# Kernel optimization log

Hardware: AMD Instinct MI355X
Metric: run time of the kernel (lower is better)

## Reference

```python
import jax, jax.numpy as jnp
import numpy as np

WS = 7       # window size
SHIFT = 3    # shift size (ws // 2)
NH = 8       # num heads


def _make_swin_mask(Hp, Wp, ws, shift):
    # Standard Swin attn mask for shifted windows: (nW, ws*ws, ws*ws)
    img = np.zeros((Hp, Wp), dtype=np.float32)
    cnt = 0
    for hs in (slice(0, -ws), slice(-ws, -shift), slice(-shift, None)):
        for wsl in (slice(0, -ws), slice(-ws, -shift), slice(-shift, None)):
            img[hs, wsl] = cnt
            cnt += 1
    mw = img.reshape(Hp // ws, ws, Wp // ws, ws).transpose(0, 2, 1, 3).reshape(-1, ws * ws)
    diff = mw[:, None, :] - mw[:, :, None]
    return jnp.asarray(np.where(diff != 0, -100.0, 0.0).astype(np.float32))


def setup_inputs() -> dict:
    key = jax.random.key(0)
    ks = jax.random.split(key, 5)
    B, H, W, C = 8, 128, 128, 256
    pad = (WS - H % WS) % WS
    Hp, Wp = H + pad, W + pad  # 133, 133
    x = jax.random.normal(ks[0], (B, H * W, C), dtype=jnp.float32)
    qkv_w = jax.random.normal(ks[1], (3 * C, C), dtype=jnp.float32) * 0.02
    qkv_b = jax.random.normal(ks[2], (3 * C,), dtype=jnp.float32) * 0.02
    proj_w = jax.random.normal(ks[3], (C, C), dtype=jnp.float32) * 0.02
    proj_b = jax.random.normal(ks[4], (C,), dtype=jnp.float32) * 0.02
    mask_matrix = _make_swin_mask(Hp, Wp, WS, SHIFT)
    return {"x": x, "qkv_w": qkv_w, "qkv_b": qkv_b, "proj_w": proj_w,
            "proj_b": proj_b, "mask_matrix": mask_matrix, "H": H, "W": W}


def reference(x, qkv_w, qkv_b, proj_w, proj_b, mask_matrix, H, W):
    B, N, C = x.shape
    hd = C // NH
    scale = hd ** -0.5
    xg = x.reshape(B, H, W, C)
    pad_r = (WS - W % WS) % WS
    pad_b = (WS - H % WS) % WS
    xg = jnp.pad(xg, ((0, 0), (0, pad_b), (0, pad_r), (0, 0)))
    Hp, Wp = H + pad_b, W + pad_r
    xg = jnp.roll(xg, (-SHIFT, -SHIFT), axis=(1, 2))
    h, w = Hp // WS, Wp // WS
    nW = h * w
    wsws = WS * WS
    # window partition -> (B*nW, wsws, C)
    xw = xg.reshape(B, h, WS, w, WS, C).transpose(0, 1, 3, 2, 4, 5).reshape(B * nW, wsws, C)
    qkv = xw @ qkv_w.T + qkv_b                       # (B*nW, wsws, 3C)
    qkv = qkv.reshape(B * nW, wsws, 3, NH, hd).transpose(2, 0, 3, 1, 4)
    q, k, v = qkv[0], qkv[1], qkv[2]                 # (B*nW, NH, wsws, hd)
    attn = jnp.einsum('bhqd,bhkd->bhqk', q, k) * scale
    attn = attn.reshape(B, nW, NH, wsws, wsws) + mask_matrix[None, :, None]
    attn = jax.nn.softmax(attn, axis=-1).reshape(B * nW, NH, wsws, wsws)
    out = jnp.einsum('bhqk,bhkd->bhqd', attn, v)
    out = out.transpose(0, 2, 1, 3).reshape(B * nW, wsws, C)
    out = out @ proj_w.T + proj_b
    # window reverse -> (B, Hp, Wp, C)
    out = out.reshape(B, h, w, WS, WS, C).transpose(0, 1, 3, 2, 4, 5).reshape(B, Hp, Wp, C)
    out = jnp.roll(out, (SHIFT, SHIFT), axis=(1, 2))
    return out[:, :H, :W, :].reshape(B, N, C)
```

## Files before the change

kernel.cpp:

```cpp
#include <hip/hip_runtime.h>
#include <hip/hip_bf16.h>
#include <cstdint>
#include <cstddef>

#define WS7    7
#define NHEADS 8
#define HD     32
#define CDIM   256
#define HP     133
#define NWY    19
#define NWIN   361
#define BATCH  8
#define HIMG   128
#define TOK    49
#define MTOK   64

typedef __attribute__((ext_vector_type(8))) short short8;
typedef __attribute__((ext_vector_type(4))) short short4v;
typedef __attribute__((ext_vector_type(4))) float f32x4;

#define XROW 264
#define VROW 72
#define VT_OFF     33792
#define SMEM_BYTES 70656

__device__ __forceinline__ short f2bf(float f) {
  union { float f; uint32_t u; } v; v.f = f;
  uint32_t r = v.u + 0x7FFFu + ((v.u >> 16) & 1u);
  return (short)(r >> 16);
}

#if defined(__has_builtin)
#if __has_builtin(__builtin_amdgcn_mfma_f32_16x16x16bf16_1k)
#define HAVE_MFMA16 1
#endif
#endif

__device__ __forceinline__ f32x4 mfma16(short4v a, short4v b, f32x4 c) {
#ifdef HAVE_MFMA16
  return __builtin_amdgcn_mfma_f32_16x16x16bf16_1k(a, b, c, 0, 0, 0);
#else
  asm("v_mfma_f32_16x16x16_bf16 %0, %1, %2, %0" : "+v"(c) : "v"(a), "v"(b));
  return c;
#endif
}

__device__ __forceinline__ short4v cvt4(f32x4 v, f32x4 b, float sc) {
  return (short4v){ f2bf((v[0] + b[0]) * sc), f2bf((v[1] + b[1]) * sc),
                    f2bf((v[2] + b[2]) * sc), f2bf((v[3] + b[3]) * sc) };
}

__device__ __forceinline__ int regcode(int c) { return (c < 126) ? 0 : ((c < 130) ? 1 : 2); }

__global__ void cvt_weights(const float* __restrict__ qkv_w, const float* __restrict__ proj_w,
                            short* __restrict__ qkvw_bf, short* __restrict__ projw_bf) {
  int stride = gridDim.x * blockDim.x;
  int i0 = blockIdx.x * blockDim.x + threadIdx.x;
  for (int i = i0; i < 768 * 256; i += stride) qkvw_bf[i] = f2bf(qkv_w[i]);
  for (int i = i0; i < 256 * 256; i += stride) projw_bf[i] = f2bf(proj_w[i]);
}

__global__ __launch_bounds__(512, 4) void swin_fused(
    const float* __restrict__ x, const short* __restrict__ qkvw,
    const float* __restrict__ qkv_b, const short* __restrict__ projw,
    const float* __restrict__ proj_b, float* __restrict__ out)
{
  extern __shared__ char smem[];
  const int tid  = threadIdx.x;
  const int wave = tid >> 6;
  const int lane = tid & 63;
  const int lg   = lane >> 4;
  const int ln   = lane & 15;
  const int blk  = blockIdx.x;
  const int b    = blk / NWIN;
  const int wdx  = blk - b * NWIN;
  const int wy   = wdx / NWY;
  const int wx   = wdx - wy * NWY;

  for (int i = tid; i < MTOK * 64; i += 512) {
    int r  = i >> 6;
    int c4 = i & 63;
    short4v v = (short4v){0, 0, 0, 0};
    if (r < TOK) {
      int ty = r / WS7, tx = r - (r / WS7) * WS7;
      int sh = wy * WS7 + ty + 3; if (sh >= HP) sh -= HP;
      int sw = wx * WS7 + tx + 3; if (sw >= HP) sw -= HP;
      if (sh < HIMG && sw < HIMG) {
        const float4* p = reinterpret_cast<const float4*>(
            x + (((size_t)b * (HIMG * HIMG) + (size_t)sh * HIMG + sw) * CDIM + c4 * 4));
        float4 f = *p;
        v = (short4v){f2bf(f.x), f2bf(f.y), f2bf(f.z), f2bf(f.w)};
      }
    }
    *reinterpret_cast<short4v*>(smem + ((size_t)r * XROW + c4 * 4) * 2) = v;
  }
  __syncthreads();

  const int h = wave;
  const int qcol = h * HD;
  const int kcol = 256 + h * HD;
  const int vcol = 512 + h * HD;
  const float scale = 0.17677669529663687f;

  f32x4 acc[2][4];
  short4v qf[2][4], kf[2][4];

#pragma unroll
  for (int ct = 0; ct < 2; ++ct)
#pragma unroll
    for (int tt = 0; tt < 4; ++tt) acc[ct][tt] = (f32x4){0, 0, 0, 0};
#pragma unroll 2
  for (int ks = 0; ks < 8; ++ks) {
    int k0 = ks * 32 + lg * 8;
    short8 xb[4];
#pragma unroll
    for (int tt = 0; tt < 4; ++tt)
      xb[tt] = *reinterpret_cast<const short8*>(smem + ((16 * tt + ln) * XROW + k0) * 2);
    short8 w[2];
#pragma unroll
    for (int ct = 0; ct < 2; ++ct)
      w[ct] = *reinterpret_cast<const short8*>(qkvw + (size_t)(qcol + 16 * ct + ln) * CDIM + k0);
#pragma unroll
    for (int ct = 0; ct < 2; ++ct)
#pragma unroll
      for (int tt = 0; tt < 4; ++tt)
        acc[ct][tt] = __builtin_amdgcn_mfma_f32_16x16x32_bf16(w[ct], xb[tt], acc[ct][tt], 0, 0, 0);
  }
#pragma unroll
  for (int ct = 0; ct < 2; ++ct) {
    f32x4 bias = *reinterpret_cast<const f32x4*>(qkv_b + qcol + 16 * ct + 4 * lg);
#pragma unroll
    for (int tt = 0; tt < 4; ++tt) qf[ct][tt] = cvt4(acc[ct][tt], bias, scale);
  }

#pragma unroll
  for (int ct = 0; ct < 2; ++ct)
#pragma unroll
    for (int tt = 0; tt < 4; ++tt) acc[ct][tt] = (f32x4){0, 0, 0, 0};
#pragma unroll 2
  for (int ks = 0; ks < 8; ++ks) {
    int k0 = ks * 32 + lg * 8;
    short8 xb[4];
#pragma unroll
    for (int tt = 0; tt < 4; ++tt)
      xb[tt] = *reinterpret_cast<const short8*>(smem + ((16 * tt + ln) * XROW + k0) * 2);
    short8 w[2];
#pragma unroll
    for (int ct = 0; ct < 2; ++ct)
      w[ct] = *reinterpret_cast<const short8*>(qkvw + (size_t)(kcol + 16 * ct + ln) * CDIM + k0);
#pragma unroll
    for (int ct = 0; ct < 2; ++ct)
#pragma unroll
      for (int tt = 0; tt < 4; ++tt)
        acc[ct][tt] = __builtin_amdgcn_mfma_f32_16x16x32_bf16(w[ct], xb[tt], acc[ct][tt], 0, 0, 0);
  }
#pragma unroll
  for (int ct = 0; ct < 2; ++ct) {
    f32x4 bias = *reinterpret_cast<const f32x4*>(qkv_b + kcol + 16 * ct + 4 * lg);
#pragma unroll
    for (int tt = 0; tt < 4; ++tt) kf[ct][tt] = cvt4(acc[ct][tt], bias, 1.0f);
  }

#pragma unroll
  for (int ct = 0; ct < 2; ++ct)
#pragma unroll
    for (int tt = 0; tt < 4; ++tt) acc[ct][tt] = (f32x4){0, 0, 0, 0};
#pragma unroll 2
  for (int ks = 0; ks < 8; ++ks) {
    int k0 = ks * 32 + lg * 8;
    short8 xb[4];
#pragma unroll
    for (int tt = 0; tt < 4; ++tt)
      xb[tt] = *reinterpret_cast<const short8*>(smem + ((16 * tt + ln) * XROW + k0) * 2);
    short8 w[2];
#pragma unroll
    for (int ct = 0; ct < 2; ++ct)
      w[ct] = *reinterpret_cast<const short8*>(qkvw + (size_t)(vcol + 16 * ct + ln) * CDIM + k0);
#pragma unroll
    for (int ct = 0; ct < 2; ++ct)
#pragma unroll
      for (int tt = 0; tt < 4; ++tt)
        acc[ct][tt] = __builtin_amdgcn_mfma_f32_16x16x32_bf16(w[ct], xb[tt], acc[ct][tt], 0, 0, 0);
  }
#pragma unroll
  for (int ct = 0; ct < 2; ++ct) {
    f32x4 bias = *reinterpret_cast<const f32x4*>(qkv_b + vcol + 16 * ct + 4 * lg);
#pragma unroll
    for (int tt = 0; tt < 4; ++tt)
#pragma unroll
      for (int r = 0; r < 4; ++r) {
        int row = h * HD + 16 * ct + 4 * lg + r;
        int col = 16 * tt + ln;
        *reinterpret_cast<short*>(smem + VT_OFF + (row * VROW + col) * 2) =
            f2bf(acc[ct][tt][r] + bias[r]);
      }
  }
  __syncthreads();

  f32x4 s[4][4];
#pragma unroll
  for (int kt = 0; kt < 4; ++kt)
#pragma unroll
    for (int qt = 0; qt < 4; ++qt) s[kt][qt] = (f32x4){0, 0, 0, 0};
#pragma unroll
  for (int step = 0; step < 2; ++step)
#pragma unroll
    for (int kt = 0; kt < 4; ++kt)
#pragma unroll
      for (int qt = 0; qt < 4; ++qt)
        s[kt][qt] = mfma16(kf[step][kt], qf[step][qt], s[kt][qt]);

  const bool bnd = (wy == NWY - 1) || (wx == NWY - 1);
  short4v pf[4][4];
#pragma unroll
  for (int qt = 0; qt < 4; ++qt) {
    int q = 16 * qt + ln;
    int qcode = 0;
    if (bnd) {
      int qy = (q * 37) >> 8, qx = q - 7 * qy;
      qcode = 3 * regcode(wy * WS7 + qy) + regcode(wx * WS7 + qx);
    }
#pragma unroll
    for (int kt = 0; kt < 4; ++kt)
#pragma unroll
      for (int r = 0; r < 4; ++r) {
        int key = 16 * kt + 4 * lg + r;
        float v = s[kt][qt][r];
        if (bnd) {
          int ky = (key * 37) >> 8, kx = key - 7 * ky;
          int kc = 3 * regcode(wy * WS7 + ky) + regcode(wx * WS7 + kx);
          if (kc != qcode) v -= 100.0f;
        }
        if (key >= TOK) v = -1e30f;
        s[kt][qt][r] = v;
      }
    float m = -1e30f;
#pragma unroll
    for (int kt = 0; kt < 4; ++kt)
#pragma unroll
      for (int r = 0; r < 4; ++r) m = fmaxf(m, s[kt][qt][r]);
    m = fmaxf(m, __shfl_xor(m, 16));
    m = fmaxf(m, __shfl_xor(m, 32));
    float sum = 0.f;
#pragma unroll
    for (int kt = 0; kt < 4; ++kt)
#pragma unroll
      for (int r = 0; r < 4; ++r) {
        float e = __expf(s[kt][qt][r] - m);
        s[kt][qt][r] = e; sum += e;
      }
    sum += __shfl_xor(sum, 16);
    sum += __shfl_xor(sum, 32);
    float inv = 1.0f / sum;
#pragma unroll
    for (int kt = 0; kt < 4; ++kt)
      pf[kt][qt] = (short4v){ f2bf(s[kt][qt][0] * inv), f2bf(s[kt][qt][1] * inv),
                              f2bf(s[kt][qt][2] * inv), f2bf(s[kt][qt][3] * inv) };
  }

  f32x4 o[4][2];
#pragma unroll
  for (int qt = 0; qt < 4; ++qt)
#pragma unroll
    for (int n2 = 0; n2 < 2; ++n2) o[qt][n2] = (f32x4){0, 0, 0, 0};
#pragma unroll
  for (int kt = 0; kt < 4; ++kt) {
    short4v vb0 = *reinterpret_cast<const short4v*>(
        smem + VT_OFF + ((h * HD + ln) * VROW + 16 * kt + 4 * lg) * 2);
    short4v vb1 = *reinterpret_cast<const short4v*>(
        smem + VT_OFF + ((h * HD + 16 + ln) * VROW + 16 * kt + 4 * lg) * 2);
#pragma unroll
    for (int qt = 0; qt < 4; ++qt) {
      o[qt][0] = mfma16(pf[kt][qt], vb0, o[qt][0]);
      o[qt][1] = mfma16(pf[kt][qt], vb1, o[qt][1]);
    }
  }

#pragma unroll
  for (int qt = 0; qt < 4; ++qt)
#pragma unroll
    for (int n2 = 0; n2 < 2; ++n2)
#pragma unroll
      for (int r = 0; r < 4; ++r) {
        int row = 16 * qt + 4 * lg + r;
        int col = h * HD + 16 * n2 + ln;
        *reinterpret_cast<short*>(smem + (row * XROW + col) * 2) = f2bf(o[qt][n2][r]);
      }
  __syncthreads();

  f32x4 pacc[4][2];
#pragma unroll
  for (int mt = 0; mt < 4; ++mt)
#pragma unroll
    for (int n2 = 0; n2 < 2; ++n2) pacc[mt][n2] = (f32x4){0, 0, 0, 0};
#pragma unroll 2
  for (int ks = 0; ks < 8; ++ks) {
    int k0 = ks * 32 + lg * 8;
    short8 afr[4];
#pragma unroll
    for (int mt = 0; mt < 4; ++mt)
      afr[mt] = *reinterpret_cast<const short8*>(smem + ((16 * mt + ln) * XROW + k0) * 2);
    short8 bfr[2];
#pragma unroll
    for (int n2 = 0; n2 < 2; ++n2)
      bfr[n2] = *reinterpret_cast<const short8*>(projw + (size_t)(h * HD + 16 * n2 + ln) * CDIM + k0);
#pragma unroll
    for (int n2 = 0; n2 < 2; ++n2)
#pragma unroll
      for (int mt = 0; mt < 4; ++mt)
        pacc[mt][n2] = __builtin_amdgcn_mfma_f32_16x16x32_bf16(afr[mt], bfr[n2], pacc[mt][n2], 0, 0, 0);
  }

  float pb0 = proj_b[h * HD + ln];
  float pb1 = proj_b[h * HD + 16 + ln];
#pragma unroll
  for (int mt = 0; mt < 4; ++mt)
#pragma unroll
    for (int r = 0; r < 4; ++r) {
      int t = 16 * mt + 4 * lg + r;
      if (t < TOK) {
        int ty = t / WS7, tx = t - (t / WS7) * WS7;
        int sh = wy * WS7 + ty + 3; if (sh >= HP) sh -= HP;
        int sw = wx * WS7 + tx + 3; if (sw >= HP) sw -= HP;
        if (sh < HIMG && sw < HIMG) {
          float* po = out + ((size_t)b * (HIMG * HIMG) + (size_t)sh * HIMG + sw) * CDIM + h * HD + ln;
          po[0]  = pacc[mt][0][r] + pb0;
          po[16] = pacc[mt][1][r] + pb1;
        }
      }
    }
}

extern "C" void kernel_launch(void* const* d_in, const int* in_sizes, int n_in,
                              void* d_out, int out_size, void* d_ws, size_t ws_size,
                              hipStream_t stream) {
  const float* x      = (const float*)d_in[0];
  const float* qkv_w  = (const float*)d_in[1];
  const float* qkv_b  = (const float*)d_in[2];
  const float* proj_w = (const float*)d_in[3];
  const float* proj_b = (const float*)d_in[4];
  float* out          = (float*)d_out;

  short* qkvw_bf = (short*)d_ws;
  short* projw_bf = (short*)((char*)d_ws + 768 * 256 * 2);

  hipLaunchKernelGGL(cvt_weights, dim3(256), dim3(256), 0, stream,
                     qkv_w, proj_w, qkvw_bf, projw_bf);

  hipFuncSetAttribute((const void*)swin_fused,
                      hipFuncAttributeMaxDynamicSharedMemorySize, SMEM_BYTES);
  hipLaunchKernelGGL(swin_fused, dim3(BATCH * NWIN), dim3(512), SMEM_BYTES, stream,
                     x, qkvw_bf, qkv_b, projw_bf, proj_b, out);
}
```

Baseline: 273.7 us.

## Use packed bf16 conversion, exp2 softmax, and permuted V and output layouts

Replaces scalar bf16 rounding with the packed hardware conversion, and folds log2(e) into the query scale and mask constant so softmax can use exp2. Restructures the x load so each wave loads whole rows. Changes the V transpose padding and interleaves head-dim columns so the attention output is written as packed 32-bit stores. The aim is fewer conversion and exponent instructions and fewer shared-memory stores, at the cost of a more intricate column permutation that must stay consistent across stages.

```diff
diff --git a/kernel.cpp b/kernel.cpp
--- a/kernel.cpp
+++ b/kernel.cpp
@@ -14,21 +14,41 @@
 #define HIMG   128
 #define TOK    49
 #define MTOK   64
+#define SHIFT3 3
 
 typedef __attribute__((ext_vector_type(8))) short short8;
 typedef __attribute__((ext_vector_type(4))) short short4v;
 typedef __attribute__((ext_vector_type(4))) float f32x4;
 
-#define XROW 264
-#define VROW 72
-#define VT_OFF     33792
-#define SMEM_BYTES 70656
+#define XROWB  528
+#define VROW   76
+#define VT_OFF 33792
+#define SMEM_BYTES (VT_OFF + 256*VROW*2)
+
+#define QS      0.25505653712988137f
+#define MASKL2 -144.26950408889634f
 
 __device__ __forceinline__ short f2bf(float f) {
   union { float f; uint32_t u; } v; v.f = f;
   uint32_t r = v.u + 0x7FFFu + ((v.u >> 16) & 1u);
   return (short)(r >> 16);
 }
+
+__device__ __forceinline__ uint32_t pk2(float a, float b) {
+  union { __hip_bfloat162 h; uint32_t u; } cv;
+  cv.h = __float22bfloat162_rn(float2{a, b});
+  return cv.u;
+}
+
+#if defined(__has_builtin)
+#if __has_builtin(__builtin_amdgcn_exp2f)
+#define EXP2F __builtin_amdgcn_exp2f
+#else
+#define EXP2F exp2f
+#endif
+#else
+#define EXP2F exp2f
+#endif
 
 #if defined(__has_builtin)
 #if __has_builtin(__builtin_amdgcn_mfma_f32_16x16x16bf16_1k)
@@ -43,11 +63,6 @@
   asm("v_mfma_f32_16x16x16_bf16 %0, %1, %2, %0" : "+v"(c) : "v"(a), "v"(b));
   return c;
 #endif
-}
-
-__device__ __forceinline__ short4v cvt4(f32x4 v, f32x4 b, float sc) {
-  return (short4v){ f2bf((v[0] + b[0]) * sc), f2bf((v[1] + b[1]) * sc),
-                    f2bf((v[2] + b[2]) * sc), f2bf((v[3] + b[3]) * sc) };
 }
 
 __device__ __forceinline__ int regcode(int c) { return (c < 126) ? 0 : ((c < 130) ? 1 : 2); }
@@ -77,22 +92,24 @@
   const int wy   = wdx / NWY;
   const int wx   = wdx - wy * NWY;
 
-  for (int i = tid; i < MTOK * 64; i += 512) {
-    int r  = i >> 6;
-    int c4 = i & 63;
-    short4v v = (short4v){0, 0, 0, 0};
-    if (r < TOK) {
-      int ty = r / WS7, tx = r - (r / WS7) * WS7;
-      int sh = wy * WS7 + ty + 3; if (sh >= HP) sh -= HP;
-      int sw = wx * WS7 + tx + 3; if (sw >= HP) sw -= HP;
-      if (sh < HIMG && sw < HIMG) {
-        const float4* p = reinterpret_cast<const float4*>(
-            x + (((size_t)b * (HIMG * HIMG) + (size_t)sh * HIMG + sw) * CDIM + c4 * 4));
-        float4 f = *p;
-        v = (short4v){f2bf(f.x), f2bf(f.y), f2bf(f.z), f2bf(f.w)};
+  {
+    const int c4 = lane;
+#pragma unroll
+    for (int it = 0; it < 8; ++it) {
+      int r = 8 * it + wave;
+      uint2 v = make_uint2(0u, 0u);
+      if (r < TOK) {
+        int ty = r / WS7, tx = r - WS7 * (r / WS7);
+        int sh = wy * WS7 + ty + SHIFT3; if (sh >= HP) sh -= HP;
+        int sw = wx * WS7 + tx + SHIFT3; if (sw >= HP) sw -= HP;
+        if (sh < HIMG && sw < HIMG) {
+          const float4 f = *reinterpret_cast<const float4*>(
+              x + (((size_t)b * (HIMG * HIMG) + sh * HIMG + sw) * CDIM + c4 * 4));
+          v = make_uint2(pk2(f.x, f.y), pk2(f.z, f.w));
+        }
       }
-    }
-    *reinterpret_cast<short4v*>(smem + ((size_t)r * XROW + c4 * 4) * 2) = v;
+      *reinterpret_cast<uint2*>(smem + r * XROWB + c4 * 8) = v;
+    }
   }
   __syncthreads();
 
@@ -100,100 +117,78 @@
   const int qcol = h * HD;
   const int kcol = 256 + h * HD;
   const int vcol = 512 + h * HD;
-  const float scale = 0.17677669529663687f;
 
   f32x4 acc[2][4];
   short4v qf[2][4], kf[2][4];
 
-#pragma unroll
-  for (int ct = 0; ct < 2; ++ct)
-#pragma unroll
-    for (int tt = 0; tt < 4; ++tt) acc[ct][tt] = (f32x4){0, 0, 0, 0};
-#pragma unroll 2
-  for (int ks = 0; ks < 8; ++ks) {
-    int k0 = ks * 32 + lg * 8;
-    short8 xb[4];
-#pragma unroll
-    for (int tt = 0; tt < 4; ++tt)
-      xb[tt] = *reinterpret_cast<const short8*>(smem + ((16 * tt + ln) * XROW + k0) * 2);
-    short8 w[2];
-#pragma unroll
-    for (int ct = 0; ct < 2; ++ct)
-      w[ct] = *reinterpret_cast<const short8*>(qkvw + (size_t)(qcol + 16 * ct + ln) * CDIM + k0);
-#pragma unroll
-    for (int ct = 0; ct < 2; ++ct)
-#pragma unroll
-      for (int tt = 0; tt < 4; ++tt)
-        acc[ct][tt] = __builtin_amdgcn_mfma_f32_16x16x32_bf16(w[ct], xb[tt], acc[ct][tt], 0, 0, 0);
-  }
+#define QKV_PASS(COLBASE)                                                          \
+  _Pragma("unroll")                                                                \
+  for (int ct = 0; ct < 2; ++ct)                                                   \
+    _Pragma("unroll")                                                              \
+    for (int tt = 0; tt < 4; ++tt) acc[ct][tt] = (f32x4){0, 0, 0, 0};              \
+  _Pragma("unroll 2")                                                              \
+  for (int ks = 0; ks < 8; ++ks) {                                                 \
+    const int k0 = ks * 32 + lg * 8;                                               \
+    short8 xb[4];                                                                  \
+    _Pragma("unroll")                                                              \
+    for (int tt = 0; tt < 4; ++tt)                                                 \
+      xb[tt] = *reinterpret_cast<const short8*>(smem + (16 * tt + ln) * XROWB + k0 * 2); \
+    short8 w[2];                                                                   \
+    _Pragma("unroll")                                                              \
+    for (int ct = 0; ct < 2; ++ct)                                                 \
+      w[ct] = *reinterpret_cast<const short8*>(qkvw + (size_t)((COLBASE) + 16 * ct + ln) * CDIM + k0); \
+    _Pragma("unroll")                                                              \
+    for (int ct = 0; ct < 2; ++ct)                                                 \
+      _Pragma("unroll")                                                            \
+      for (int tt = 0; tt < 4; ++tt)                                               \
+        acc[ct][tt] = __builtin_amdgcn_mfma_f32_16x16x32_bf16(w[ct], xb[tt], acc[ct][tt], 0, 0, 0); \
+  }
+
+  QKV_PASS(qcol)
 #pragma unroll
   for (int ct = 0; ct < 2; ++ct) {
     f32x4 bias = *reinterpret_cast<const f32x4*>(qkv_b + qcol + 16 * ct + 4 * lg);
 #pragma unroll
-    for (int tt = 0; tt < 4; ++tt) qf[ct][tt] = cvt4(acc[ct][tt], bias, scale);
-  }
-
-#pragma unroll
-  for (int ct = 0; ct < 2; ++ct)
-#pragma unroll
-    for (int tt = 0; tt < 4; ++tt) acc[ct][tt] = (f32x4){0, 0, 0, 0};
-#pragma unroll 2
-  for (int ks = 0; ks < 8; ++ks) {
-    int k0 = ks * 32 + lg * 8;
-    short8 xb[4];
-#pragma unroll
-    for (int tt = 0; tt < 4; ++tt)
-      xb[tt] = *reinterpret_cast<const short8*>(smem + ((16 * tt + ln) * XROW + k0) * 2);
-    short8 w[2];
-#pragma unroll
-    for (int ct = 0; ct < 2; ++ct)
-      w[ct] = *reinterpret_cast<const short8*>(qkvw + (size_t)(kcol + 16 * ct + ln) * CDIM + k0);
-#pragma unroll
-    for (int ct = 0; ct < 2; ++ct)
-#pragma unroll
-      for (int tt = 0; tt < 4; ++tt)
-        acc[ct][tt] = __builtin_amdgcn_mfma_f32_16x16x32_bf16(w[ct], xb[tt], acc[ct][tt], 0, 0, 0);
-  }
+    for (int tt = 0; tt < 4; ++tt) {
+      float e0 = fmaf(acc[ct][tt][0], QS, bias[0] * QS);
+      float e1 = fmaf(acc[ct][tt][1], QS, bias[1] * QS);
+      float e2 = fmaf(acc[ct][tt][2], QS, bias[2] * QS);
+      float e3 = fmaf(acc[ct][tt][3], QS, bias[3] * QS);
+      union { uint2 u; short4v s; } cv;
+      cv.u = make_uint2(pk2(e0, e1), pk2(e2, e3));
+      qf[ct][tt] = cv.s;
+    }
+  }
+
+  QKV_PASS(kcol)
 #pragma unroll
   for (int ct = 0; ct < 2; ++ct) {
     f32x4 bias = *reinterpret_cast<const f32x4*>(qkv_b + kcol + 16 * ct + 4 * lg);
 #pragma unroll
-    for (int tt = 0; tt < 4; ++tt) kf[ct][tt] = cvt4(acc[ct][tt], bias, 1.0f);
-  }
-
-#pragma unroll
-  for (int ct = 0; ct < 2; ++ct)
-#pragma unroll
-    for (int tt = 0; tt < 4; ++tt) acc[ct][tt] = (f32x4){0, 0, 0, 0};
-#pragma unroll 2
-  for (int ks = 0; ks < 8; ++ks) {
-    int k0 = ks * 32 + lg * 8;
-    short8 xb[4];
-#pragma unroll
-    for (int tt = 0; tt < 4; ++tt)
-      xb[tt] = *reinterpret_cast<const short8*>(smem + ((16 * tt + ln) * XROW + k0) * 2);
-    short8 w[2];
-#pragma unroll
-    for (int ct = 0; ct < 2; ++ct)
-      w[ct] = *reinterpret_cast<const short8*>(qkvw + (size_t)(vcol + 16 * ct + ln) * CDIM + k0);
-#pragma unroll
-    for (int ct = 0; ct < 2; ++ct)
-#pragma unroll
-      for (int tt = 0; tt < 4; ++tt)
-        acc[ct][tt] = __builtin_amdgcn_mfma_f32_16x16x32_bf16(w[ct], xb[tt], acc[ct][tt], 0, 0, 0);
-  }
+    for (int tt = 0; tt < 4; ++tt) {
+      union { uint2 u; short4v s; } cv;
+      cv.u = make_uint2(pk2(acc[ct][tt][0] + bias[0], acc[ct][tt][1] + bias[1]),
+                        pk2(acc[ct][tt][2] + bias[2], acc[ct][tt][3] + bias[3]));
+      kf[ct][tt] = cv.s;
+    }
+  }
+
+  QKV_PASS(vcol)
 #pragma unroll
   for (int ct = 0; ct < 2; ++ct) {
     f32x4 bias = *reinterpret_cast<const f32x4*>(qkv_b + vcol + 16 * ct + 4 * lg);
 #pragma unroll
-    for (int tt = 0; tt < 4; ++tt)
-#pragma unroll
-      for (int r = 0; r < 4; ++r) {
-        int row = h * HD + 16 * ct + 4 * lg + r;
-        int col = 16 * tt + ln;
-        *reinterpret_cast<short*>(smem + VT_OFF + (row * VROW + col) * 2) =
-            f2bf(acc[ct][tt][r] + bias[r]);
-      }
+    for (int tt = 0; tt < 4; ++tt) {
+      uint32_t p01 = pk2(acc[ct][tt][0] + bias[0], acc[ct][tt][1] + bias[1]);
+      uint32_t p23 = pk2(acc[ct][tt][2] + bias[2], acc[ct][tt][3] + bias[3]);
+      int row0 = h * HD + 16 * ct + 4 * lg;
+      int col  = 16 * tt + ln;
+      char* base = smem + VT_OFF + (row0 * VROW + col) * 2;
+      *reinterpret_cast<short*>(base)            = (short)(p01 & 0xFFFF);
+      *reinterpret_cast<short*>(base + VROW * 2) = (short)(p01 >> 16);
+      *reinterpret_cast<short*>(base + VROW * 4) = (short)(p23 & 0xFFFF);
+      *reinterpret_cast<short*>(base + VROW * 6) = (short)(p23 >> 16);
+    }
   }
   __syncthreads();
 
@@ -217,7 +212,7 @@
     int q = 16 * qt + ln;
     int qcode = 0;
     if (bnd) {
-      int qy = (q * 37) >> 8, qx = q - 7 * qy;
+      int qy = q / WS7, qx = q - WS7 * (q / WS7);
       qcode = 3 * regcode(wy * WS7 + qy) + regcode(wx * WS7 + qx);
     }
 #pragma unroll
@@ -227,9 +222,9 @@
         int key = 16 * kt + 4 * lg + r;
         float v = s[kt][qt][r];
         if (bnd) {
-          int ky = (key * 37) >> 8, kx = key - 7 * ky;
+          int ky = key / WS7, kx = key - WS7 * (key / WS7);
           int kc = 3 * regcode(wy * WS7 + ky) + regcode(wx * WS7 + kx);
-          if (kc != qcode) v -= 100.0f;
+          v += (kc != qcode) ? MASKL2 : 0.f;
         }
         if (key >= TOK) v = -1e30f;
         s[kt][qt][r] = v;
@@ -246,16 +241,19 @@
     for (int kt = 0; kt < 4; ++kt)
 #pragma unroll
       for (int r = 0; r < 4; ++r) {
-        float e = __expf(s[kt][qt][r] - m);
+        float e = EXP2F(s[kt][qt][r] - m);
         s[kt][qt][r] = e; sum += e;
       }
     sum += __shfl_xor(sum, 16);
     sum += __shfl_xor(sum, 32);
     float inv = 1.0f / sum;
 #pragma unroll
-    for (int kt = 0; kt < 4; ++kt)
-      pf[kt][qt] = (short4v){ f2bf(s[kt][qt][0] * inv), f2bf(s[kt][qt][1] * inv),
-                              f2bf(s[kt][qt][2] * inv), f2bf(s[kt][qt][3] * inv) };
+    for (int kt = 0; kt < 4; ++kt) {
+      union { uint2 u; short4v sv; } cv;
+      cv.u = make_uint2(pk2(s[kt][qt][0] * inv, s[kt][qt][1] * inv),
+                        pk2(s[kt][qt][2] * inv, s[kt][qt][3] * inv));
+      pf[kt][qt] = cv.sv;
+    }
   }
 
   f32x4 o[4][2];
@@ -265,10 +263,11 @@
     for (int n2 = 0; n2 < 2; ++n2) o[qt][n2] = (f32x4){0, 0, 0, 0};
 #pragma unroll
   for (int kt = 0; kt < 4; ++kt) {
+    int tok = 16 * kt + 4 * lg;
     short4v vb0 = *reinterpret_cast<const short4v*>(
-        smem + VT_OFF + ((h * HD + ln) * VROW + 16 * kt + 4 * lg) * 2);
+        smem + VT_OFF + ((h * HD + 2 * ln) * VROW + tok) * 2);
     short4v vb1 = *reinterpret_cast<const short4v*>(
-        smem + VT_OFF + ((h * HD + 16 + ln) * VROW + 16 * kt + 4 * lg) * 2);
+        smem + VT_OFF + ((h * HD + 2 * ln + 1) * VROW + tok) * 2);
 #pragma unroll
     for (int qt = 0; qt < 4; ++qt) {
       o[qt][0] = mfma16(pf[kt][qt], vb0, o[qt][0]);
@@ -279,13 +278,11 @@
 #pragma unroll
   for (int qt = 0; qt < 4; ++qt)
 #pragma unroll
-    for (int n2 = 0; n2 < 2; ++n2)
-#pragma unroll
-      for (int r = 0; r < 4; ++r) {
-        int row = 16 * qt + 4 * lg + r;
-        int col = h * HD + 16 * n2 + ln;
-        *reinterpret_cast<short*>(smem + (row * XROW + col) * 2) = f2bf(o[qt][n2][r]);
-      }
+    for (int r = 0; r < 4; ++r) {
+      int row = 16 * qt + 4 * lg + r;
+      uint32_t p = pk2(o[qt][0][r], o[qt][1][r]);
+      *reinterpret_cast<uint32_t*>(smem + row * XROWB + h * 64 + 4 * ln) = p;
+    }
   __syncthreads();
 
   f32x4 pacc[4][2];
@@ -299,7 +296,7 @@
     short8 afr[4];
 #pragma unroll
     for (int mt = 0; mt < 4; ++mt)
-      afr[mt] = *reinterpret_cast<const short8*>(smem + ((16 * mt + ln) * XROW + k0) * 2);
+      afr[mt] = *reinterpret_cast<const short8*>(smem + (16 * mt + ln) * XROWB + k0 * 2);
     short8 bfr[2];
 #pragma unroll
     for (int n2 = 0; n2 < 2; ++n2)
@@ -319,11 +316,11 @@
     for (int r = 0; r < 4; ++r) {
       int t = 16 * mt + 4 * lg + r;
       if (t < TOK) {
-        int ty = t / WS7, tx = t - (t / WS7) * WS7;
-        int sh = wy * WS7 + ty + 3; if (sh >= HP) sh -= HP;
-        int sw = wx * WS7 + tx + 3; if (sw >= HP) sw -= HP;
+        int ty = t / WS7, tx = t - WS7 * (t / WS7);
+        int sh = wy * WS7 + ty + SHIFT3; if (sh >= HP) sh -= HP;
+        int sw = wx * WS7 + tx + SHIFT3; if (sw >= HP) sw -= HP;
         if (sh < HIMG && sw < HIMG) {
-          float* po = out + ((size_t)b * (HIMG * HIMG) + (size_t)sh * HIMG + sw) * CDIM + h * HD + ln;
+          float* po = out + ((size_t)b * (HIMG * HIMG) + sh * HIMG + sw) * CDIM + h * HD + ln;
           po[0]  = pacc[mt][0][r] + pb0;
           po[16] = pacc[mt][1][r] + pb1;
         }
```

Result: no change. 270.0 us (-1.4%).
